# Kernel optimization log

Measured on AMD Instinct MI355X. Metric: run time of the kernel, lower is better.

The kernel has to match this reference:

```python
import jax, jax.numpy as jnp
import numpy as np

H = 4096      # hidden_size
NH = 32       # num query heads
NKV = 2       # multi_query_group_num (kv heads)
HD = 128      # head_dim
ROT = 64      # rotary_dim = head_dim // 2
B, S = 2, 2048
QKV = (NH + 2 * NKV) * HD  # 4608
BASE = 10000.0


def apply_rope(x, pos):
    """GPT-J style (non-neox, interleaved) rope on first ROT dims of head_dim.
    x: [B,S,n,HD], pos: [B,S] int."""
    half = ROT // 2  # 32 frequency pairs
    inv_freq = 1.0 / (BASE ** (jnp.arange(0, ROT, 2, dtype=jnp.float32) / ROT))  # [half]
    freqs = pos.astype(jnp.float32)[..., None] * inv_freq        # [B,S,half]
    cos = jnp.cos(freqs)[:, :, None, :]                          # [B,S,1,half]
    sin = jnp.sin(freqs)[:, :, None, :]
    xr, xp = x[..., :ROT], x[..., ROT:]
    x1 = xr[..., 0::2]   # [B,S,n,half]
    x2 = xr[..., 1::2]
    o1 = x1 * cos - x2 * sin
    o2 = x2 * cos + x1 * sin
    rot = jnp.stack([o1, o2], axis=-1).reshape(x.shape[:-1] + (ROT,))
    return jnp.concatenate([rot, xp], axis=-1)


def setup_inputs() -> dict:
    key = jax.random.key(0)
    k1, k2, k3, k4 = jax.random.split(key, 4)
    hidden_states = jax.random.normal(k1, (B, S, H), dtype=jnp.float32)
    position_ids = jnp.broadcast_to(jnp.arange(S, dtype=jnp.int64), (B, S))
    Wqkv = jax.random.normal(k2, (H, QKV), dtype=jnp.float32) * 0.02
    bqkv = jax.random.normal(k3, (QKV,), dtype=jnp.float32) * 0.02
    Wo = jax.random.normal(k4, (NH * HD, H), dtype=jnp.float32) * 0.02
    return {"hidden_states": hidden_states, "position_ids": position_ids,
            "Wqkv": Wqkv, "bqkv": bqkv, "Wo": Wo}


def reference(hidden_states, position_ids, Wqkv, bqkv, Wo):
    qkv = hidden_states @ Wqkv + bqkv                      # [B,S,QKV]
    q = qkv[..., : NH * HD].reshape(B, S, NH, HD)
    k = qkv[..., NH * HD : (NH + NKV) * HD].reshape(B, S, NKV, HD)
    v = qkv[..., (NH + NKV) * HD :].reshape(B, S, NKV, HD)

    q = apply_rope(q, position_ids)
    k = apply_rope(k, position_ids)

    # GQA: expand kv heads to match query heads
    rep = NH // NKV
    k = jnp.repeat(k, rep, axis=2)   # [B,S,NH,HD]
    v = jnp.repeat(v, rep, axis=2)

    scale = HD ** -0.5
    scores = jnp.einsum("bqhd,bkhd->bhqk", q, k) * scale   # [B,NH,S,S]
    causal = jnp.tril(jnp.ones((S, S), dtype=bool))
    scores = jnp.where(causal, scores, jnp.finfo(scores.dtype).min)
    probs = jax.nn.softmax(scores, axis=-1)
    ctx = jnp.einsum("bhqk,bkhd->bqhd", probs, v).reshape(B, S, NH * HD)
    return ctx @ Wo                                        # [B,S,H]
```

## Files before the change

### kernel.cpp

```cpp
#include <hip/hip_runtime.h>
#include <stdint.h>

#define B_    2
#define S_    2048
#define H_    4096
#define NH_   32
#define NKV_  2
#define HD_   128
#define ROT_  64
#define QKVD  4608
#define MROWS 4096

typedef __attribute__((ext_vector_type(8))) __bf16 bf16x8;
typedef __attribute__((ext_vector_type(4))) float f32x4;

__device__ __forceinline__ unsigned short f2bf(float f) {
    union { float f; unsigned u; } c; c.f = f;
    unsigned u = c.u;
    u += 0x7fffu + ((u >> 16) & 1u);
    return (unsigned short)(u >> 16);
}

__device__ __forceinline__ void gload_lds16(const void* g, void* l) {
    __builtin_amdgcn_global_load_lds(
        (__attribute__((address_space(1))) void*)g,
        (__attribute__((address_space(3))) void*)l, 16, 0, 0);
}

__global__ __launch_bounds__(256) void convert_bf16(const float* __restrict__ src,
                                                    unsigned short* __restrict__ dst,
                                                    int n4) {
    int i = blockIdx.x * 256 + threadIdx.x;
    if (i < n4) {
        f32x4 v = ((const f32x4*)src)[i];
        ushort4 o;
        o.x = f2bf(v[0]); o.y = f2bf(v[1]); o.z = f2bf(v[2]); o.w = f2bf(v[3]);
        ((ushort4*)dst)[i] = o;
    }
}

__global__ __launch_bounds__(256) void transpose_bf16(const float* __restrict__ src,
                                                      unsigned short* __restrict__ dst,
                                                      int K, int N) {
    __shared__ float tile[32][33];
    int n0 = blockIdx.x * 32, k0 = blockIdx.y * 32;
    int tx = threadIdx.x & 31, ty = threadIdx.x >> 5;
#pragma unroll
    for (int i = 0; i < 4; i++)
        tile[ty + i * 8][tx] = src[(size_t)(k0 + ty + i * 8) * N + n0 + tx];
    __syncthreads();
#pragma unroll
    for (int i = 0; i < 4; i++)
        dst[(size_t)(n0 + ty + i * 8) * K + k0 + tx] = f2bf(tile[tx][ty + i * 8]);
}


__device__ __forceinline__ void stage_half(const unsigned short* g,
                                           unsigned short* slot,
                                           int kt, int tid, int wave) {
    int ko = (kt < 64 ? kt : 63) << 6;
#pragma unroll
    for (int j = 0; j < 2; j++) {
        int li = j * 512 + tid;
        int r = li >> 3, s = li & 7;
        gload_lds16(g + ((size_t)r << 12) + ko + ((s ^ (r & 7)) << 3),
                    slot + (size_t)(j * 512 + wave * 64) * 8);
    }
}

template <int PAR, int MH>
__device__ __forceinline__ void lda_frags(const unsigned short* lds, bf16x8 (&af)[4][2],
                                          int wm, int lrow, int quad, int lw) {
    const unsigned short* p = lds + (PAR * 2 + MH) * 8192 + (wm * 64 + lrow) * 64;
#pragma unroll
    for (int mf = 0; mf < 4; mf++)
#pragma unroll
        for (int ks = 0; ks < 2; ks++)
            af[mf][ks] = *(const bf16x8*)(p + mf * 1024 + (((ks * 4 + quad) ^ lw) << 3));
}

template <int PAR, int NH>
__device__ __forceinline__ void ldb_frags(const unsigned short* lds, bf16x8 (&bf)[2][2],
                                          int wn, int lrow, int quad, int lw) {
    const unsigned short* p =
        lds + 32768 + (PAR * 2 + NH) * 8192 + (wn * 32 + lrow) * 64;
#pragma unroll
    for (int nf = 0; nf < 2; nf++)
#pragma unroll
        for (int ks = 0; ks < 2; ks++)
            bf[nf][ks] = *(const bf16x8*)(p + nf * 1024 + (((ks * 4 + quad) ^ lw) << 3));
}

template <int MH, int NH>
__device__ __forceinline__ void mfma_quad(f32x4 (&acc)[8][4], const bf16x8 (&af)[4][2],
                                          const bf16x8 (&bf)[2][2]) {
#pragma unroll
    for (int mf = 0; mf < 4; mf++)
#pragma unroll
        for (int nf = 0; nf < 2; nf++)
#pragma unroll
            for (int ks = 0; ks < 2; ks++)
                acc[MH * 4 + mf][NH * 2 + nf] = __builtin_amdgcn_mfma_f32_16x16x32_bf16(
                    af[mf][ks], bf[nf][ks], acc[MH * 4 + mf][NH * 2 + nf], 0, 0, 0);
}

#define MMPH(MH, NH, BF)                                   \
    __builtin_amdgcn_s_barrier();                          \
    asm volatile("s_waitcnt lgkmcnt(0)" ::: "memory");     \
    __builtin_amdgcn_s_setprio(1);                         \
    mfma_quad<MH, NH>(acc, af, BF);                        \
    __builtin_amdgcn_s_setprio(0);

template <int EPI, int N>
__global__ __launch_bounds__(512, 2) void gemm256(const unsigned short* __restrict__ A,
                                                  const unsigned short* __restrict__ BT,
                                                  const float* __restrict__ bias,
                                                  float* __restrict__ C,
                                                  unsigned short* __restrict__ Qb,
                                                  unsigned short* __restrict__ Kb,
                                                  unsigned short* __restrict__ Vb) {
    extern __shared__ unsigned short lds[];
    const int tid = threadIdx.x;
    const int lane = tid & 63, wave = tid >> 6;
    const int wm = wave >> 2, wn = wave & 3;
    const int quad = lane >> 4, lrow = lane & 15, lw = lrow & 7;
    const int m0 = blockIdx.y * 256, n0 = blockIdx.x * 256;
    const unsigned short* gA0 = A + ((size_t)m0 << 12);
    const unsigned short* gA1 = gA0 + ((size_t)128 << 12);
    const unsigned short* gB0 = BT + ((size_t)n0 << 12);
    const unsigned short* gB1 = gB0 + ((size_t)128 << 12);

    f32x4 acc[8][4];
#pragma unroll
    for (int i = 0; i < 8; i++)
#pragma unroll
        for (int j = 0; j < 4; j++) acc[i][j] = (f32x4){0.f, 0.f, 0.f, 0.f};
    bf16x8 af[4][2], bf0[2][2], bf1[2][2];

    stage_half(gA0, lds,                 0, tid, wave);
    stage_half(gB0, lds + 32768,         0, tid, wave);
    stage_half(gA1, lds + 8192,          0, tid, wave);
    stage_half(gB1, lds + 32768 + 8192,  0, tid, wave);
    stage_half(gA0, lds + 16384,         1, tid, wave);
    stage_half(gB0, lds + 32768 + 16384, 1, tid, wave);
    asm volatile("s_waitcnt vmcnt(4)" ::: "memory");
    __builtin_amdgcn_s_barrier();

#pragma unroll 1
    for (int i = 0; i < 32; ++i) {
        const int t0 = 2 * i;
        lda_frags<0, 0>(lds, af, wm, lrow, quad, lw);
        ldb_frags<0, 0>(lds, bf0, wn, lrow, quad, lw);
        stage_half(gA1, lds + 24576, t0 + 1, tid, wave);
        MMPH(0, 0, bf0);
        __builtin_amdgcn_s_barrier();
        ldb_frags<0, 1>(lds, bf1, wn, lrow, quad, lw);
        stage_half(gB1, lds + 32768 + 24576, t0 + 1, tid, wave);
        MMPH(0, 1, bf1);
        __builtin_amdgcn_s_barrier();
        lda_frags<0, 1>(lds, af, wm, lrow, quad, lw);
        stage_half(gA0, lds, t0 + 2, tid, wave);
        MMPH(1, 0, bf0);
        __builtin_amdgcn_s_barrier();
        stage_half(gB0, lds + 32768, t0 + 2, tid, wave);
        MMPH(1, 1, bf1);
        asm volatile("s_waitcnt vmcnt(4)" ::: "memory");
        __builtin_amdgcn_s_barrier();
        lda_frags<1, 0>(lds, af, wm, lrow, quad, lw);
        ldb_frags<1, 0>(lds, bf0, wn, lrow, quad, lw);
        stage_half(gA1, lds + 8192, t0 + 2, tid, wave);
        MMPH(0, 0, bf0);
        __builtin_amdgcn_s_barrier();
        ldb_frags<1, 1>(lds, bf1, wn, lrow, quad, lw);
        stage_half(gB1, lds + 32768 + 8192, t0 + 2, tid, wave);
        MMPH(0, 1, bf1);
        __builtin_amdgcn_s_barrier();
        lda_frags<1, 1>(lds, af, wm, lrow, quad, lw);
        stage_half(gA0, lds + 16384, t0 + 3, tid, wave);
        MMPH(1, 0, bf0);
        __builtin_amdgcn_s_barrier();
        stage_half(gB0, lds + 32768 + 16384, t0 + 3, tid, wave);
        MMPH(1, 1, bf1);
        asm volatile("s_waitcnt vmcnt(4)" ::: "memory");
        __builtin_amdgcn_s_barrier();
    }

    if constexpr (EPI == 0) {
#pragma unroll
        for (int mh = 0; mh < 2; mh++)
#pragma unroll
            for (int mf = 0; mf < 4; mf++) {
                int gm = m0 + mh * 128 + wm * 64 + mf * 16 + quad * 4;
#pragma unroll
                for (int nh = 0; nh < 2; nh++)
#pragma unroll
                    for (int nf = 0; nf < 2; nf++) {
                        int gn = n0 + nh * 128 + wn * 32 + nf * 16 + lrow;
#pragma unroll
                        for (int r = 0; r < 4; r++)
                            C[(size_t)(gm + r) * N + gn] = acc[mh * 4 + mf][nh * 2 + nf][r];
                    }
            }
    } else {
        const float QSCALE = 0.08838834764831843f * 1.4426950408889634f;
#pragma unroll
        for (int mh = 0; mh < 2; mh++)
#pragma unroll
            for (int mf = 0; mf < 4; mf++) {
                int gm = m0 + mh * 128 + wm * 64 + mf * 16 + quad * 4;
                int bb = gm >> 11;
                int srow = gm & (S_ - 1);
#pragma unroll
                for (int nh = 0; nh < 2; nh++)
#pragma unroll
                    for (int nf = 0; nf < 2; nf++) {
                        int colF = n0 + nh * 128 + wn * 32 + nf * 16 + lrow;
                        int head = colF >> 7, dcol = colF & 127;
                        float bv = bias[colF];
                        float vals[4];
#pragma unroll
                        for (int r = 0; r < 4; r++)
                            vals[r] = acc[mh * 4 + mf][nh * 2 + nf][r] + bv;
                        if (head < 34 && dcol < ROT_) {
                            int p = dcol >> 1;
                            float inv = exp2f(-(float)p * 0.41524101186092035f);
                            int odd = dcol & 1;
#pragma unroll
                            for (int r = 0; r < 4; r++) {
                                float partner = __shfl_xor(vals[r], 1);
                                float sn, cs;
                                __sincosf((float)(srow + r) * inv, &sn, &cs);
                                vals[r] = odd ? (vals[r] * cs + partner * sn)
                                              : (vals[r] * cs - partner * sn);
                            }
                        }
                        if (head < 32) {
                            unsigned short* dst =
                                Qb + ((size_t)(bb * NH_ + head) * S_ + srow) * HD_ + dcol;
#pragma unroll
                            for (int r = 0; r < 4; r++) dst[r * HD_] = f2bf(vals[r] * QSCALE);
                        } else if (head < 34) {
                            size_t base = ((size_t)(bb * NKV_ + head - 32) * S_ + srow) * HD_;
#pragma unroll
                            for (int r = 0; r < 4; r++)
                                Kb[base + r * HD_ + (((dcol >> 3) ^ ((srow + r) & 7)) << 3) +
                                   (dcol & 7)] = f2bf(vals[r]);
                        } else {
                            size_t base = ((size_t)(bb * NKV_ + head - 34) * HD_ + dcol) * S_;
#pragma unroll
                            for (int r = 0; r < 4; r++) {
                                int s = srow + r;
                                Vb[base + ((s >> 6) << 6) +
                                   ((((s >> 3) & 7) ^ (dcol & 7)) << 3) + (s & 7)] =
                                    f2bf(vals[r]);
                            }
                        }
                    }
            }
    }
}
#undef MMPH

__global__ __launch_bounds__(256, 4) void flash4(const unsigned short* __restrict__ Qb,
                                                 const unsigned short* __restrict__ Kb,
                                                 const unsigned short* __restrict__ Vb,
                                                 unsigned short* __restrict__ ctxb) {
    int pair = blockIdx.x;
    int h = blockIdx.y, b = blockIdx.z;
    int tid = threadIdx.x, lane = tid & 63, wave = tid >> 6;
    int quad = lane >> 4, lrow = lane & 15;
    int bkvh = b * NKV_ + (h >> 4);
    int lw3 = lrow & 7;

    __shared__ __align__(16) unsigned short Ks[64 * 128];
    __shared__ __align__(16) unsigned short Vt[128 * 64];
    __shared__ __align__(16) unsigned short Ps[4][16 * 64];

    const unsigned short* Kg = Kb + (size_t)bkvh * S_ * HD_;
    const unsigned short* Vg = Vb + (size_t)bkvh * HD_ * S_;

#pragma unroll 1
    for (int u = 0; u < 2; u++) {
        int qblk = u ? ((int)(S_ / 64) - 1 - pair) : pair;
        int q0 = qblk * 64 + wave * 16;

        bf16x8 qf[4];
        {
            const unsigned short* qr =
                Qb + ((size_t)(b * NH_ + h) * S_ + q0 + lrow) * HD_ + quad * 8;
#pragma unroll
            for (int c = 0; c < 4; c++) qf[c] = *(const bf16x8*)(qr + c * 32);
        }

        float m_i[4], l_i[4];
        f32x4 oacc[8];
#pragma unroll
        for (int r = 0; r < 4; r++) { m_i[r] = -1e30f; l_i[r] = 0.f; }
#pragma unroll
        for (int t = 0; t < 8; t++) oacc[t] = (f32x4){0.f, 0.f, 0.f, 0.f};

        int nkt = qblk + 1;
#pragma unroll 1
        for (int kt = 0; kt < nkt; kt++) {
            int ks0 = kt * 64;
            {
                const unsigned short* g =
                    Kg + (size_t)(ks0 + wave * 16 + (lane >> 4)) * HD_ + (lane & 15) * 8;
                unsigned short* l = &Ks[wave * 16 * 128];
#pragma unroll
                for (int i = 0; i < 4; i++)
                    gload_lds16(g + i * 4 * 128, l + i * 4 * 128);
            }
            {
                const unsigned short* g =
                    Vg + (size_t)(wave * 32 + (lane >> 3)) * S_ + ks0 + (lane & 7) * 8;
                unsigned short* l = &Vt[wave * 32 * 64];
#pragma unroll
                for (int i = 0; i < 4; i++)
                    gload_lds16(g + (size_t)i * 8 * S_, l + i * 8 * 64);
            }
            __syncthreads();

            if (ks0 <= q0 + 15) {
                f32x4 s[4];
#pragma unroll
                for (int n = 0; n < 4; n++) s[n] = (f32x4){0.f, 0.f, 0.f, 0.f};
#pragma unroll
                for (int kc = 0; kc < 4; kc++)
#pragma unroll
                    for (int n = 0; n < 4; n++) {
                        bf16x8 kf = *(const bf16x8*)
                            &Ks[(n * 16 + lrow) * 128 + (((kc * 4 + quad) ^ lw3) << 3)];
                        s[n] = __builtin_amdgcn_mfma_f32_16x16x32_bf16(qf[kc], kf, s[n],
                                                                       0, 0, 0);
                    }
                if (kt == nkt - 1) {
#pragma unroll
                    for (int n = 0; n < 4; n++)
#pragma unroll
                        for (int r = 0; r < 4; r++)
                            if (ks0 + n * 16 + lrow > q0 + quad * 4 + r)
                                s[n][r] = -1e30f;
                }
                float alpha[4];
#pragma unroll
                for (int r = 0; r < 4; r++) {
                    float mx = fmaxf(fmaxf(s[0][r], s[1][r]), fmaxf(s[2][r], s[3][r]));
                    mx = fmaxf(mx, __shfl_xor(mx, 1));
                    mx = fmaxf(mx, __shfl_xor(mx, 2));
                    mx = fmaxf(mx, __shfl_xor(mx, 4));
                    mx = fmaxf(mx, __shfl_xor(mx, 8));
                    float mn = fmaxf(m_i[r], mx);
                    alpha[r] = exp2f(m_i[r] - mn);
                    m_i[r] = mn;
                    float rs = 0.f;
#pragma unroll
                    for (int n = 0; n < 4; n++) {
                        s[n][r] = exp2f(s[n][r] - mn);
                        rs += s[n][r];
                    }
                    rs += __shfl_xor(rs, 1);
                    rs += __shfl_xor(rs, 2);
                    rs += __shfl_xor(rs, 4);
                    rs += __shfl_xor(rs, 8);
                    l_i[r] = l_i[r] * alpha[r] + rs;
                }
#pragma unroll
                for (int n = 0; n < 4; n++)
#pragma unroll
                    for (int r = 0; r < 4; r++) {
                        int rw = quad * 4 + r, col = n * 16 + lrow;
                        Ps[wave][rw * 64 + (((col >> 3) ^ (rw & 7)) << 3) + (col & 7)] =
                            f2bf(s[n][r]);
                    }
#pragma unroll
                for (int t = 0; t < 8; t++)
#pragma unroll
                    for (int r = 0; r < 4; r++) oacc[t][r] *= alpha[r];
                bf16x8 pf0 = *(const bf16x8*)&Ps[wave][lrow * 64 + ((quad ^ lw3) << 3)];
                bf16x8 pf1 = *(const bf16x8*)&Ps[wave][lrow * 64 + (((4 + quad) ^ lw3) << 3)];
#pragma unroll
                for (int t = 0; t < 8; t++) {
                    int dim = t * 16 + lrow;
                    bf16x8 v0 = *(const bf16x8*)&Vt[dim * 64 + ((quad ^ lw3) << 3)];
                    bf16x8 v1 = *(const bf16x8*)&Vt[dim * 64 + (((4 + quad) ^ lw3) << 3)];
                    oacc[t] = __builtin_amdgcn_mfma_f32_16x16x32_bf16(pf0, v0, oacc[t], 0, 0, 0);
                    oacc[t] = __builtin_amdgcn_mfma_f32_16x16x32_bf16(pf1, v1, oacc[t], 0, 0, 0);
                }
            }
            __syncthreads();
        }
        float inv[4];
#pragma unroll
        for (int r = 0; r < 4; r++) inv[r] = 1.f / l_i[r];
#pragma unroll
        for (int t = 0; t < 8; t++)
#pragma unroll
            for (int r = 0; r < 4; r++) {
                int q = q0 + quad * 4 + r;
                ctxb[(size_t)(b * S_ + q) * (NH_ * HD_) + h * HD_ + t * 16 + lrow] =
                    f2bf(oacc[t][r] * inv[r]);
            }
    }
}

extern "C" void kernel_launch(void* const* d_in, const int* in_sizes, int n_in,
                              void* d_out, int out_size, void* d_ws, size_t ws_size,
                              hipStream_t stream) {
    const float* hidden = (const float*)d_in[0];
    const float* Wqkv = (const float*)d_in[2];
    const float* bqkv = (const float*)d_in[3];
    const float* Wo   = (const float*)d_in[4];
    float* out = (float*)d_out;

    char* ws = (char*)d_ws;
    unsigned short* Xb    = (unsigned short*)ws;
    unsigned short* WqkvT = (unsigned short*)(ws + 33554432);
    unsigned short* Qb    = (unsigned short*)(ws + 71303168);
    unsigned short* Kb    = (unsigned short*)(ws + 104857600);
    unsigned short* Vb    = (unsigned short*)(ws + 106954752);
    unsigned short* ctxb  = (unsigned short*)(ws + 109051904);
    unsigned short* WoT   = Xb;

    convert_bf16<<<16384, 256, 0, stream>>>(hidden, Xb, (MROWS * H_) / 4);
    transpose_bf16<<<dim3(QKVD / 32, H_ / 32), 256, 0, stream>>>(Wqkv, WqkvT, H_, QKVD);
    gemm256<1, QKVD><<<dim3(QKVD / 256, MROWS / 256), 512, 131072, stream>>>(
        Xb, WqkvT, bqkv, nullptr, Qb, Kb, Vb);
    transpose_bf16<<<dim3(H_ / 32, H_ / 32), 256, 0, stream>>>(Wo, WoT, NH_ * HD_, H_);
    flash4<<<dim3(S_ / 128, NH_, B_), 256, 0, stream>>>(Qb, Kb, Vb, ctxb);
    gemm256<0, H_><<<dim3(H_ / 256, MROWS / 256), 512, 131072, stream>>>(
        ctxb, WoT, nullptr, out, nullptr, nullptr, nullptr);
}
```

Baseline: 711.2 us.

## Double-buffer 32-key K/V tiles in flash attention and remap GEMM block order

Rewrites the attention kernel to use 32-key tiles with double-buffered K/V loads into LDS. The next tile's load is issued before computing the current one, using vmcnt waits and raw barriers instead of __syncthreads, to overlap global loads with MFMA work. The V layout written by the QKV GEMM epilogue is changed to contiguous 32-key chunks with a new swizzle, so each tile loads as one contiguous 8 KB block. The GEMM also remaps block IDs in an XCD-aware order for cache locality. Smaller tiles double the loop iterations and the barrier count per query block.

```diff
diff --git a/kernel.cpp b/kernel.cpp
--- a/kernel.cpp
+++ b/kernel.cpp
@@ -124,7 +124,11 @@
     const int lane = tid & 63, wave = tid >> 6;
     const int wm = wave >> 2, wn = wave & 3;
     const int quad = lane >> 4, lrow = lane & 15, lw = lrow & 7;
-    const int m0 = blockIdx.y * 256, n0 = blockIdx.x * 256;
+    const int nx = gridDim.x;
+    const int bid0 = blockIdx.y * nx + blockIdx.x;
+    const int cpx = (nx * gridDim.y) >> 3;
+    const int bid = (bid0 & 7) * cpx + (bid0 >> 3);
+    const int m0 = (bid / nx) * 256, n0 = (bid % nx) * 256;
     const unsigned short* gA0 = A + ((size_t)m0 << 12);
     const unsigned short* gA1 = gA0 + ((size_t)128 << 12);
     const unsigned short* gB0 = BT + ((size_t)n0 << 12);
@@ -246,12 +250,12 @@
                                 Kb[base + r * HD_ + (((dcol >> 3) ^ ((srow + r) & 7)) << 3) +
                                    (dcol & 7)] = f2bf(vals[r]);
                         } else {
-                            size_t base = ((size_t)(bb * NKV_ + head - 34) * HD_ + dcol) * S_;
+                            size_t base = (size_t)(bb * NKV_ + head - 34) * S_ * HD_;
 #pragma unroll
                             for (int r = 0; r < 4; r++) {
                                 int s = srow + r;
-                                Vb[base + ((s >> 6) << 6) +
-                                   ((((s >> 3) & 7) ^ (dcol & 7)) << 3) + (s & 7)] =
+                                Vb[base + (size_t)(s >> 5) * 4096 + dcol * 32 +
+                                   ((((s >> 3) & 3) ^ ((dcol >> 1) & 3)) << 3) + (s & 7)] =
                                     f2bf(vals[r]);
                             }
                         }
@@ -261,7 +265,7 @@
 }
 #undef MMPH
 
-__global__ __launch_bounds__(256, 4) void flash4(const unsigned short* __restrict__ Qb,
+__global__ __launch_bounds__(256, 4) void flash5(const unsigned short* __restrict__ Qb,
                                                  const unsigned short* __restrict__ Kb,
                                                  const unsigned short* __restrict__ Vb,
                                                  unsigned short* __restrict__ ctxb) {
@@ -272,16 +276,16 @@
     int bkvh = b * NKV_ + (h >> 4);
     int lw3 = lrow & 7;
 
-    __shared__ __align__(16) unsigned short Ks[64 * 128];
-    __shared__ __align__(16) unsigned short Vt[128 * 64];
-    __shared__ __align__(16) unsigned short Ps[4][16 * 64];
+    __shared__ __align__(16) unsigned short Ks[2][32 * 128];
+    __shared__ __align__(16) unsigned short Vt[2][128 * 32];
+    __shared__ __align__(16) unsigned short Ps[4][16 * 32];
 
     const unsigned short* Kg = Kb + (size_t)bkvh * S_ * HD_;
-    const unsigned short* Vg = Vb + (size_t)bkvh * HD_ * S_;
+    const unsigned short* Vg = Vb + (size_t)bkvh * S_ * HD_;
 
 #pragma unroll 1
     for (int u = 0; u < 2; u++) {
-        int qblk = u ? ((int)(S_ / 64) - 1 - pair) : pair;
+        int qblk = u ? (31 - pair) : pair;
         int q0 = qblk * 64 + wave * 16;
 
         bf16x8 qf[4];
@@ -299,53 +303,60 @@
 #pragma unroll
         for (int t = 0; t < 8; t++) oacc[t] = (f32x4){0.f, 0.f, 0.f, 0.f};
 
-        int nkt = qblk + 1;
+        int nkt = 2 * qblk + 2;
+        gload_lds16(Kg + tid * 8, &Ks[0][tid * 8]);
+        gload_lds16(Kg + (256 + tid) * 8, &Ks[0][(256 + tid) * 8]);
+        gload_lds16(Vg + tid * 8, &Vt[0][tid * 8]);
+        gload_lds16(Vg + (256 + tid) * 8, &Vt[0][(256 + tid) * 8]);
+
 #pragma unroll 1
         for (int kt = 0; kt < nkt; kt++) {
-            int ks0 = kt * 64;
-            {
-                const unsigned short* g =
-                    Kg + (size_t)(ks0 + wave * 16 + (lane >> 4)) * HD_ + (lane & 15) * 8;
-                unsigned short* l = &Ks[wave * 16 * 128];
-#pragma unroll
-                for (int i = 0; i < 4; i++)
-                    gload_lds16(g + i * 4 * 128, l + i * 4 * 128);
+            int cur = kt & 1;
+            if (kt + 1 < nkt) {
+                const unsigned short* gk = Kg + (size_t)(kt + 1) * 4096;
+                const unsigned short* gv = Vg + (size_t)(kt + 1) * 4096;
+                int nb = cur ^ 1;
+                gload_lds16(gk + tid * 8, &Ks[nb][tid * 8]);
+                gload_lds16(gk + (256 + tid) * 8, &Ks[nb][(256 + tid) * 8]);
+                gload_lds16(gv + tid * 8, &Vt[nb][tid * 8]);
+                gload_lds16(gv + (256 + tid) * 8, &Vt[nb][(256 + tid) * 8]);
+                asm volatile("s_waitcnt vmcnt(4)" ::: "memory");
+            } else {
+                asm volatile("s_waitcnt vmcnt(0)" ::: "memory");
             }
-            {
-                const unsigned short* g =
-                    Vg + (size_t)(wave * 32 + (lane >> 3)) * S_ + ks0 + (lane & 7) * 8;
-                unsigned short* l = &Vt[wave * 32 * 64];
-#pragma unroll
-                for (int i = 0; i < 4; i++)
-                    gload_lds16(g + (size_t)i * 8 * S_, l + i * 8 * 64);
-            }
-            __syncthreads();
-
+            __builtin_amdgcn_s_barrier();
+            asm volatile("" ::: "memory");
+
+            int ks0 = kt * 32;
             if (ks0 <= q0 + 15) {
-                f32x4 s[4];
-#pragma unroll
-                for (int n = 0; n < 4; n++) s[n] = (f32x4){0.f, 0.f, 0.f, 0.f};
+                const unsigned short* KsB = &Ks[cur][0];
+                const unsigned short* VtB = &Vt[cur][0];
+                f32x4 s2[2];
+                s2[0] = (f32x4){0.f, 0.f, 0.f, 0.f};
+                s2[1] = (f32x4){0.f, 0.f, 0.f, 0.f};
+                __builtin_amdgcn_s_setprio(1);
 #pragma unroll
                 for (int kc = 0; kc < 4; kc++)
 #pragma unroll
-                    for (int n = 0; n < 4; n++) {
+                    for (int n = 0; n < 2; n++) {
                         bf16x8 kf = *(const bf16x8*)
-                            &Ks[(n * 16 + lrow) * 128 + (((kc * 4 + quad) ^ lw3) << 3)];
-                        s[n] = __builtin_amdgcn_mfma_f32_16x16x32_bf16(qf[kc], kf, s[n],
-                                                                       0, 0, 0);
+                            &KsB[(n * 16 + lrow) * 128 + (((kc * 4 + quad) ^ lw3) << 3)];
+                        s2[n] = __builtin_amdgcn_mfma_f32_16x16x32_bf16(qf[kc], kf, s2[n],
+                                                                        0, 0, 0);
                     }
-                if (kt == nkt - 1) {
-#pragma unroll
-                    for (int n = 0; n < 4; n++)
+                __builtin_amdgcn_s_setprio(0);
+                if (ks0 + 31 > q0) {
+#pragma unroll
+                    for (int n = 0; n < 2; n++)
 #pragma unroll
                         for (int r = 0; r < 4; r++)
                             if (ks0 + n * 16 + lrow > q0 + quad * 4 + r)
-                                s[n][r] = -1e30f;
+                                s2[n][r] = -1e30f;
                 }
                 float alpha[4];
 #pragma unroll
                 for (int r = 0; r < 4; r++) {
-                    float mx = fmaxf(fmaxf(s[0][r], s[1][r]), fmaxf(s[2][r], s[3][r]));
+                    float mx = fmaxf(s2[0][r], s2[1][r]);
                     mx = fmaxf(mx, __shfl_xor(mx, 1));
                     mx = fmaxf(mx, __shfl_xor(mx, 2));
                     mx = fmaxf(mx, __shfl_xor(mx, 4));
@@ -355,9 +366,9 @@
                     m_i[r] = mn;
                     float rs = 0.f;
 #pragma unroll
-                    for (int n = 0; n < 4; n++) {
-                        s[n][r] = exp2f(s[n][r] - mn);
-                        rs += s[n][r];
+                    for (int n = 0; n < 2; n++) {
+                        s2[n][r] = exp2f(s2[n][r] - mn);
+                        rs += s2[n][r];
                     }
                     rs += __shfl_xor(rs, 1);
                     rs += __shfl_xor(rs, 2);
@@ -366,29 +377,33 @@
                     l_i[r] = l_i[r] * alpha[r] + rs;
                 }
 #pragma unroll
-                for (int n = 0; n < 4; n++)
+                for (int n = 0; n < 2; n++)
 #pragma unroll
                     for (int r = 0; r < 4; r++) {
                         int rw = quad * 4 + r, col = n * 16 + lrow;
-                        Ps[wave][rw * 64 + (((col >> 3) ^ (rw & 7)) << 3) + (col & 7)] =
-                            f2bf(s[n][r]);
+                        Ps[wave][rw * 32 + ((((col >> 3) ^ ((rw >> 1) & 3)) << 3)) +
+                                 (col & 7)] = f2bf(s2[n][r]);
                     }
 #pragma unroll
                 for (int t = 0; t < 8; t++)
 #pragma unroll
                     for (int r = 0; r < 4; r++) oacc[t][r] *= alpha[r];
-                bf16x8 pf0 = *(const bf16x8*)&Ps[wave][lrow * 64 + ((quad ^ lw3) << 3)];
-                bf16x8 pf1 = *(const bf16x8*)&Ps[wave][lrow * 64 + (((4 + quad) ^ lw3) << 3)];
+                bf16x8 pf = *(const bf16x8*)
+                    &Ps[wave][lrow * 32 + ((quad ^ ((lrow >> 1) & 3)) << 3)];
+                __builtin_amdgcn_s_setprio(1);
 #pragma unroll
                 for (int t = 0; t < 8; t++) {
                     int dim = t * 16 + lrow;
-                    bf16x8 v0 = *(const bf16x8*)&Vt[dim * 64 + ((quad ^ lw3) << 3)];
-                    bf16x8 v1 = *(const bf16x8*)&Vt[dim * 64 + (((4 + quad) ^ lw3) << 3)];
-                    oacc[t] = __builtin_amdgcn_mfma_f32_16x16x32_bf16(pf0, v0, oacc[t], 0, 0, 0);
-                    oacc[t] = __builtin_amdgcn_mfma_f32_16x16x32_bf16(pf1, v1, oacc[t], 0, 0, 0);
+                    bf16x8 vf = *(const bf16x8*)
+                        &VtB[dim * 32 + ((quad ^ ((dim >> 1) & 3)) << 3)];
+                    oacc[t] = __builtin_amdgcn_mfma_f32_16x16x32_bf16(pf, vf, oacc[t],
+                                                                      0, 0, 0);
                 }
+                __builtin_amdgcn_s_setprio(0);
             }
-            __syncthreads();
+            asm volatile("s_waitcnt lgkmcnt(0)" ::: "memory");
+            __builtin_amdgcn_s_barrier();
+            asm volatile("" ::: "memory");
         }
         float inv[4];
 #pragma unroll
@@ -427,7 +442,7 @@
     gemm256<1, QKVD><<<dim3(QKVD / 256, MROWS / 256), 512, 131072, stream>>>(
         Xb, WqkvT, bqkv, nullptr, Qb, Kb, Vb);
     transpose_bf16<<<dim3(H_ / 32, H_ / 32), 256, 0, stream>>>(Wo, WoT, NH_ * HD_, H_);
-    flash4<<<dim3(S_ / 128, NH_, B_), 256, 0, stream>>>(Qb, Kb, Vb, ctxb);
+    flash5<<<dim3(S_ / 128, NH_, B_), 256, 0, stream>>>(Qb, Kb, Vb, ctxb);
     gemm256<0, H_><<<dim3(H_ / 256, MROWS / 256), 512, 131072, stream>>>(
         ctxb, WoT, nullptr, out, nullptr, nullptr, nullptr);
 }
```

Measured after the change: 783.8 us. +10.2%, slower.

## Rework flash attention to 32-row waves reading K/V directly from global

Applied to the files above, without the earlier changes.

The attention kernel now gives each wave 32 query rows in two 16-row groups that share each K and V fragment, doubling MFMA work per operand load. K and V are no longer staged in shared memory: waves read them straight from global memory, which removes the block-wide barriers and lets each wave stop at its own causal limit. To make those reads simple, the QKV GEMM epilogue writes K and V without swizzling, and V is written as a plain transposed layout with vectorized 4-element stores. MFMA sections are wrapped in s_setprio. The risks are higher register pressure (launch bounds drop to 2), reliance on L1/L2 for K/V reuse, and uneven work across waves in a block.

```diff
diff --git a/kernel.cpp b/kernel.cpp
--- a/kernel.cpp
+++ b/kernel.cpp
@@ -240,20 +240,18 @@
 #pragma unroll
                             for (int r = 0; r < 4; r++) dst[r * HD_] = f2bf(vals[r] * QSCALE);
                         } else if (head < 34) {
-                            size_t base = ((size_t)(bb * NKV_ + head - 32) * S_ + srow) * HD_;
+                            size_t base =
+                                ((size_t)(bb * NKV_ + head - 32) * S_ + srow) * HD_ + dcol;
 #pragma unroll
                             for (int r = 0; r < 4; r++)
-                                Kb[base + r * HD_ + (((dcol >> 3) ^ ((srow + r) & 7)) << 3) +
-                                   (dcol & 7)] = f2bf(vals[r]);
+                                Kb[base + r * HD_] = f2bf(vals[r]);
                         } else {
-                            size_t base = ((size_t)(bb * NKV_ + head - 34) * HD_ + dcol) * S_;
-#pragma unroll
-                            for (int r = 0; r < 4; r++) {
-                                int s = srow + r;
-                                Vb[base + ((s >> 6) << 6) +
-                                   ((((s >> 3) & 7) ^ (dcol & 7)) << 3) + (s & 7)] =
-                                    f2bf(vals[r]);
-                            }
+                            size_t base =
+                                ((size_t)(bb * NKV_ + head - 34) * HD_ + dcol) * S_ + srow;
+                            ushort4 vv;
+                            vv.x = f2bf(vals[0]); vv.y = f2bf(vals[1]);
+                            vv.z = f2bf(vals[2]); vv.w = f2bf(vals[3]);
+                            *(ushort4*)&Vb[base] = vv;
                         }
                     }
             }
@@ -261,7 +259,7 @@
 }
 #undef MMPH
 
-__global__ __launch_bounds__(256, 4) void flash4(const unsigned short* __restrict__ Qb,
+__global__ __launch_bounds__(256, 2) void flash6(const unsigned short* __restrict__ Qb,
                                                  const unsigned short* __restrict__ Kb,
                                                  const unsigned short* __restrict__ Vb,
                                                  unsigned short* __restrict__ ctxb) {
@@ -272,135 +270,146 @@
     int bkvh = b * NKV_ + (h >> 4);
     int lw3 = lrow & 7;
 
-    __shared__ __align__(16) unsigned short Ks[64 * 128];
-    __shared__ __align__(16) unsigned short Vt[128 * 64];
-    __shared__ __align__(16) unsigned short Ps[4][16 * 64];
+    __shared__ __align__(16) unsigned short Ps[4][32 * 64];
 
     const unsigned short* Kg = Kb + (size_t)bkvh * S_ * HD_;
-    const unsigned short* Vg = Vb + (size_t)bkvh * HD_ * S_;
+    const unsigned short* Vg = Vb + (size_t)bkvh * S_ * HD_;
 
 #pragma unroll 1
     for (int u = 0; u < 2; u++) {
-        int qblk = u ? ((int)(S_ / 64) - 1 - pair) : pair;
-        int q0 = qblk * 64 + wave * 16;
-
-        bf16x8 qf[4];
-        {
+        int qblk = u ? (15 - pair) : pair;
+        int q0 = qblk * 128 + wave * 32;
+
+        bf16x8 qf[2][4];
+#pragma unroll
+        for (int mg = 0; mg < 2; mg++) {
             const unsigned short* qr =
-                Qb + ((size_t)(b * NH_ + h) * S_ + q0 + lrow) * HD_ + quad * 8;
-#pragma unroll
-            for (int c = 0; c < 4; c++) qf[c] = *(const bf16x8*)(qr + c * 32);
+                Qb + ((size_t)(b * NH_ + h) * S_ + q0 + mg * 16 + lrow) * HD_ + quad * 8;
+#pragma unroll
+            for (int c = 0; c < 4; c++) qf[mg][c] = *(const bf16x8*)(qr + c * 32);
         }
 
-        float m_i[4], l_i[4];
-        f32x4 oacc[8];
-#pragma unroll
-        for (int r = 0; r < 4; r++) { m_i[r] = -1e30f; l_i[r] = 0.f; }
-#pragma unroll
-        for (int t = 0; t < 8; t++) oacc[t] = (f32x4){0.f, 0.f, 0.f, 0.f};
-
-        int nkt = qblk + 1;
+        float m_i[2][4], l_i[2][4];
+        f32x4 oacc[2][8];
+#pragma unroll
+        for (int mg = 0; mg < 2; mg++) {
+#pragma unroll
+            for (int r = 0; r < 4; r++) { m_i[mg][r] = -1e30f; l_i[mg][r] = 0.f; }
+#pragma unroll
+            for (int t = 0; t < 8; t++) oacc[mg][t] = (f32x4){0.f, 0.f, 0.f, 0.f};
+        }
+
+        int nkt = qblk * 2 + (wave >> 1) + 1;
 #pragma unroll 1
         for (int kt = 0; kt < nkt; kt++) {
             int ks0 = kt * 64;
-            {
-                const unsigned short* g =
-                    Kg + (size_t)(ks0 + wave * 16 + (lane >> 4)) * HD_ + (lane & 15) * 8;
-                unsigned short* l = &Ks[wave * 16 * 128];
-#pragma unroll
-                for (int i = 0; i < 4; i++)
-                    gload_lds16(g + i * 4 * 128, l + i * 4 * 128);
-            }
-            {
-                const unsigned short* g =
-                    Vg + (size_t)(wave * 32 + (lane >> 3)) * S_ + ks0 + (lane & 7) * 8;
-                unsigned short* l = &Vt[wave * 32 * 64];
-#pragma unroll
-                for (int i = 0; i < 4; i++)
-                    gload_lds16(g + (size_t)i * 8 * S_, l + i * 8 * 64);
-            }
-            __syncthreads();
-
-            if (ks0 <= q0 + 15) {
-                f32x4 s[4];
-#pragma unroll
-                for (int n = 0; n < 4; n++) s[n] = (f32x4){0.f, 0.f, 0.f, 0.f};
-#pragma unroll
-                for (int kc = 0; kc < 4; kc++)
-#pragma unroll
-                    for (int n = 0; n < 4; n++) {
-                        bf16x8 kf = *(const bf16x8*)
-                            &Ks[(n * 16 + lrow) * 128 + (((kc * 4 + quad) ^ lw3) << 3)];
-                        s[n] = __builtin_amdgcn_mfma_f32_16x16x32_bf16(qf[kc], kf, s[n],
-                                                                       0, 0, 0);
-                    }
-                if (kt == nkt - 1) {
+            f32x4 s[2][4];
+#pragma unroll
+            for (int mg = 0; mg < 2; mg++)
+#pragma unroll
+                for (int n = 0; n < 4; n++) s[mg][n] = (f32x4){0.f, 0.f, 0.f, 0.f};
+
+            __builtin_amdgcn_s_setprio(1);
+#pragma unroll
+            for (int n = 0; n < 4; n++)
+#pragma unroll
+                for (int kc = 0; kc < 4; kc++) {
+                    bf16x8 kf = *(const bf16x8*)
+                        &Kg[(size_t)(ks0 + n * 16 + lrow) * HD_ + ((kc * 4 + quad) << 3)];
+                    s[0][n] = __builtin_amdgcn_mfma_f32_16x16x32_bf16(qf[0][kc], kf,
+                                                                      s[0][n], 0, 0, 0);
+                    s[1][n] = __builtin_amdgcn_mfma_f32_16x16x32_bf16(qf[1][kc], kf,
+                                                                      s[1][n], 0, 0, 0);
+                }
+            __builtin_amdgcn_s_setprio(0);
+
+            if (ks0 + 63 > q0) {
+#pragma unroll
+                for (int mg = 0; mg < 2; mg++)
 #pragma unroll
                     for (int n = 0; n < 4; n++)
 #pragma unroll
                         for (int r = 0; r < 4; r++)
-                            if (ks0 + n * 16 + lrow > q0 + quad * 4 + r)
-                                s[n][r] = -1e30f;
-                }
+                            if (ks0 + n * 16 + lrow > q0 + mg * 16 + quad * 4 + r)
+                                s[mg][n][r] = -1e30f;
+            }
+
+#pragma unroll
+            for (int mg = 0; mg < 2; mg++) {
                 float alpha[4];
 #pragma unroll
                 for (int r = 0; r < 4; r++) {
-                    float mx = fmaxf(fmaxf(s[0][r], s[1][r]), fmaxf(s[2][r], s[3][r]));
+                    float mx = fmaxf(fmaxf(s[mg][0][r], s[mg][1][r]),
+                                     fmaxf(s[mg][2][r], s[mg][3][r]));
                     mx = fmaxf(mx, __shfl_xor(mx, 1));
                     mx = fmaxf(mx, __shfl_xor(mx, 2));
                     mx = fmaxf(mx, __shfl_xor(mx, 4));
                     mx = fmaxf(mx, __shfl_xor(mx, 8));
-                    float mn = fmaxf(m_i[r], mx);
-                    alpha[r] = exp2f(m_i[r] - mn);
-                    m_i[r] = mn;
+                    float mn = fmaxf(m_i[mg][r], mx);
+                    alpha[r] = exp2f(m_i[mg][r] - mn);
+                    m_i[mg][r] = mn;
                     float rs = 0.f;
 #pragma unroll
                     for (int n = 0; n < 4; n++) {
-                        s[n][r] = exp2f(s[n][r] - mn);
-                        rs += s[n][r];
+                        s[mg][n][r] = exp2f(s[mg][n][r] - mn);
+                        rs += s[mg][n][r];
                     }
                     rs += __shfl_xor(rs, 1);
                     rs += __shfl_xor(rs, 2);
                     rs += __shfl_xor(rs, 4);
                     rs += __shfl_xor(rs, 8);
-                    l_i[r] = l_i[r] * alpha[r] + rs;
+                    l_i[mg][r] = l_i[mg][r] * alpha[r] + rs;
                 }
 #pragma unroll
                 for (int n = 0; n < 4; n++)
 #pragma unroll
                     for (int r = 0; r < 4; r++) {
-                        int rw = quad * 4 + r, col = n * 16 + lrow;
+                        int rw = mg * 16 + quad * 4 + r, col = n * 16 + lrow;
                         Ps[wave][rw * 64 + (((col >> 3) ^ (rw & 7)) << 3) + (col & 7)] =
-                            f2bf(s[n][r]);
+                            f2bf(s[mg][n][r]);
                     }
 #pragma unroll
                 for (int t = 0; t < 8; t++)
 #pragma unroll
-                    for (int r = 0; r < 4; r++) oacc[t][r] *= alpha[r];
-                bf16x8 pf0 = *(const bf16x8*)&Ps[wave][lrow * 64 + ((quad ^ lw3) << 3)];
-                bf16x8 pf1 = *(const bf16x8*)&Ps[wave][lrow * 64 + (((4 + quad) ^ lw3) << 3)];
-#pragma unroll
-                for (int t = 0; t < 8; t++) {
-                    int dim = t * 16 + lrow;
-                    bf16x8 v0 = *(const bf16x8*)&Vt[dim * 64 + ((quad ^ lw3) << 3)];
-                    bf16x8 v1 = *(const bf16x8*)&Vt[dim * 64 + (((4 + quad) ^ lw3) << 3)];
-                    oacc[t] = __builtin_amdgcn_mfma_f32_16x16x32_bf16(pf0, v0, oacc[t], 0, 0, 0);
-                    oacc[t] = __builtin_amdgcn_mfma_f32_16x16x32_bf16(pf1, v1, oacc[t], 0, 0, 0);
+                    for (int r = 0; r < 4; r++) oacc[mg][t][r] *= alpha[r];
+            }
+
+            bf16x8 pA[2], pB[2];
+#pragma unroll
+            for (int mg = 0; mg < 2; mg++) {
+                int prow = mg * 16 + lrow;
+                pA[mg] = *(const bf16x8*)&Ps[wave][prow * 64 + ((quad ^ lw3) << 3)];
+                pB[mg] = *(const bf16x8*)&Ps[wave][prow * 64 + (((4 + quad) ^ lw3) << 3)];
+            }
+
+            __builtin_amdgcn_s_setprio(1);
+#pragma unroll
+            for (int t = 0; t < 8; t++) {
+                int dim = t * 16 + lrow;
+                bf16x8 v0 = *(const bf16x8*)&Vg[(size_t)dim * S_ + ks0 + quad * 8];
+                bf16x8 v1 = *(const bf16x8*)&Vg[(size_t)dim * S_ + ks0 + 32 + quad * 8];
+                oacc[0][t] = __builtin_amdgcn_mfma_f32_16x16x32_bf16(pA[0], v0, oacc[0][t], 0, 0, 0);
+                oacc[0][t] = __builtin_amdgcn_mfma_f32_16x16x32_bf16(pB[0], v1, oacc[0][t], 0, 0, 0);
+                oacc[1][t] = __builtin_amdgcn_mfma_f32_16x16x32_bf16(pA[1], v0, oacc[1][t], 0, 0, 0);
+                oacc[1][t] = __builtin_amdgcn_mfma_f32_16x16x32_bf16(pB[1], v1, oacc[1][t], 0, 0, 0);
+            }
+            __builtin_amdgcn_s_setprio(0);
+        }
+
+#pragma unroll
+        for (int mg = 0; mg < 2; mg++) {
+            float inv[4];
+#pragma unroll
+            for (int r = 0; r < 4; r++) inv[r] = 1.f / l_i[mg][r];
+#pragma unroll
+            for (int t = 0; t < 8; t++)
+#pragma unroll
+                for (int r = 0; r < 4; r++) {
+                    int q = q0 + mg * 16 + quad * 4 + r;
+                    ctxb[(size_t)(b * S_ + q) * (NH_ * HD_) + h * HD_ + t * 16 + lrow] =
+                        f2bf(oacc[mg][t][r] * inv[r]);
                 }
-            }
-            __syncthreads();
         }
-        float inv[4];
-#pragma unroll
-        for (int r = 0; r < 4; r++) inv[r] = 1.f / l_i[r];
-#pragma unroll
-        for (int t = 0; t < 8; t++)
-#pragma unroll
-            for (int r = 0; r < 4; r++) {
-                int q = q0 + quad * 4 + r;
-                ctxb[(size_t)(b * S_ + q) * (NH_ * HD_) + h * HD_ + t * 16 + lrow] =
-                    f2bf(oacc[t][r] * inv[r]);
-            }
     }
 }
 
@@ -427,7 +436,7 @@
     gemm256<1, QKVD><<<dim3(QKVD / 256, MROWS / 256), 512, 131072, stream>>>(
         Xb, WqkvT, bqkv, nullptr, Qb, Kb, Vb);
     transpose_bf16<<<dim3(H_ / 32, H_ / 32), 256, 0, stream>>>(Wo, WoT, NH_ * HD_, H_);
-    flash4<<<dim3(S_ / 128, NH_, B_), 256, 0, stream>>>(Qb, Kb, Vb, ctxb);
+    flash6<<<dim3(8, NH_, B_), 256, 0, stream>>>(Qb, Kb, Vb, ctxb);
     gemm256<0, H_><<<dim3(H_ / 256, MROWS / 256), 512, 131072, stream>>>(
         ctxb, WoT, nullptr, out, nullptr, nullptr, nullptr);
 }
```

Result: slower. 807.0 us (+13.5%).

## Double-buffer GEMM register fragments to prefetch LDS reads ahead of MFMA phases

Applied to the files above, without the earlier changes.

Restructures the GEMM main loop so A and B fragments are double-buffered in registers (AF0/AF1, BF0/BF1), with LDS reads for the next phase issued before the current phase's MFMAs. The explicit lgkmcnt(0) wait inside each phase is dropped and the vmcnt gates are moved. The aim is to hide LDS read latency behind MFMA work. In exchange it raises register pressure under the 512x2 launch bound and depends on compiler-inserted waits and a reordered barrier and vmcnt schedule for correctness.

```diff
diff --git a/kernel.cpp b/kernel.cpp
--- a/kernel.cpp
+++ b/kernel.cpp
@@ -79,6 +79,17 @@
             af[mf][ks] = *(const bf16x8*)(p + mf * 1024 + (((ks * 4 + quad) ^ lw) << 3));
 }
 
+template <int PAR, int MH, int HALF>
+__device__ __forceinline__ void lda_half(const unsigned short* lds, bf16x8 (&af)[4][2],
+                                         int wm, int lrow, int quad, int lw) {
+    const unsigned short* p = lds + (PAR * 2 + MH) * 8192 + (wm * 64 + lrow) * 64;
+#pragma unroll
+    for (int mf = HALF * 2; mf < HALF * 2 + 2; mf++)
+#pragma unroll
+        for (int ks = 0; ks < 2; ks++)
+            af[mf][ks] = *(const bf16x8*)(p + mf * 1024 + (((ks * 4 + quad) ^ lw) << 3));
+}
+
 template <int PAR, int NH>
 __device__ __forceinline__ void ldb_frags(const unsigned short* lds, bf16x8 (&bf)[2][2],
                                           int wn, int lrow, int quad, int lw) {
@@ -104,12 +115,14 @@
                     af[mf][ks], bf[nf][ks], acc[MH * 4 + mf][NH * 2 + nf], 0, 0, 0);
 }
 
-#define MMPH(MH, NH, BF)                                   \
+#define MMEXEC(MH, NH, AF, BF)                             \
     __builtin_amdgcn_s_barrier();                          \
-    asm volatile("s_waitcnt lgkmcnt(0)" ::: "memory");     \
     __builtin_amdgcn_s_setprio(1);                         \
-    mfma_quad<MH, NH>(acc, af, BF);                        \
-    __builtin_amdgcn_s_setprio(0);
+    mfma_quad<MH, NH>(acc, AF, BF);                        \
+    __builtin_amdgcn_s_setprio(0);                         \
+    __builtin_amdgcn_s_barrier();
+
+#define GATE4 asm volatile("s_waitcnt vmcnt(4)" ::: "memory");
 
 template <int EPI, int N>
 __global__ __launch_bounds__(512, 2) void gemm256(const unsigned short* __restrict__ A,
@@ -135,7 +148,7 @@
     for (int i = 0; i < 8; i++)
 #pragma unroll
         for (int j = 0; j < 4; j++) acc[i][j] = (f32x4){0.f, 0.f, 0.f, 0.f};
-    bf16x8 af[4][2], bf0[2][2], bf1[2][2];
+    bf16x8 AF0[4][2], AF1[4][2], BF0[2][2], BF1[2][2];
 
     stage_half(gA0, lds,                 0, tid, wave);
     stage_half(gB0, lds + 32768,         0, tid, wave);
@@ -143,46 +156,46 @@
     stage_half(gB1, lds + 32768 + 8192,  0, tid, wave);
     stage_half(gA0, lds + 16384,         1, tid, wave);
     stage_half(gB0, lds + 32768 + 16384, 1, tid, wave);
-    asm volatile("s_waitcnt vmcnt(4)" ::: "memory");
+    GATE4
     __builtin_amdgcn_s_barrier();
+    lda_frags<0, 0>(lds, AF0, wm, lrow, quad, lw);
+    ldb_frags<0, 0>(lds, BF0, wn, lrow, quad, lw);
 
 #pragma unroll 1
     for (int i = 0; i < 32; ++i) {
         const int t0 = 2 * i;
-        lda_frags<0, 0>(lds, af, wm, lrow, quad, lw);
-        ldb_frags<0, 0>(lds, bf0, wn, lrow, quad, lw);
+        lda_half<0, 1, 0>(lds, AF1, wm, lrow, quad, lw);
+        ldb_frags<0, 1>(lds, BF1, wn, lrow, quad, lw);
         stage_half(gA1, lds + 24576, t0 + 1, tid, wave);
-        MMPH(0, 0, bf0);
-        __builtin_amdgcn_s_barrier();
-        ldb_frags<0, 1>(lds, bf1, wn, lrow, quad, lw);
+        MMEXEC(0, 0, AF0, BF0)
+        lda_half<0, 1, 1>(lds, AF1, wm, lrow, quad, lw);
         stage_half(gB1, lds + 32768 + 24576, t0 + 1, tid, wave);
-        MMPH(0, 1, bf1);
-        __builtin_amdgcn_s_barrier();
-        lda_frags<0, 1>(lds, af, wm, lrow, quad, lw);
+        GATE4
+        MMEXEC(0, 1, AF0, BF1)
+        lda_half<1, 0, 0>(lds, AF0, wm, lrow, quad, lw);
         stage_half(gA0, lds, t0 + 2, tid, wave);
-        MMPH(1, 0, bf0);
-        __builtin_amdgcn_s_barrier();
+        MMEXEC(1, 0, AF1, BF0)
+        lda_half<1, 0, 1>(lds, AF0, wm, lrow, quad, lw);
+        ldb_frags<1, 0>(lds, BF0, wn, lrow, quad, lw);
         stage_half(gB0, lds + 32768, t0 + 2, tid, wave);
-        MMPH(1, 1, bf1);
-        asm volatile("s_waitcnt vmcnt(4)" ::: "memory");
-        __builtin_amdgcn_s_barrier();
-        lda_frags<1, 0>(lds, af, wm, lrow, quad, lw);
-        ldb_frags<1, 0>(lds, bf0, wn, lrow, quad, lw);
+        GATE4
+        MMEXEC(1, 1, AF1, BF1)
+        lda_half<1, 1, 0>(lds, AF1, wm, lrow, quad, lw);
+        ldb_frags<1, 1>(lds, BF1, wn, lrow, quad, lw);
         stage_half(gA1, lds + 8192, t0 + 2, tid, wave);
-        MMPH(0, 0, bf0);
-        __builtin_amdgcn_s_barrier();
-        ldb_frags<1, 1>(lds, bf1, wn, lrow, quad, lw);
+        MMEXEC(0, 0, AF0, BF0)
+        lda_half<1, 1, 1>(lds, AF1, wm, lrow, quad, lw);
         stage_half(gB1, lds + 32768 + 8192, t0 + 2, tid, wave);
-        MMPH(0, 1, bf1);
-        __builtin_amdgcn_s_barrier();
-        lda_frags<1, 1>(lds, af, wm, lrow, quad, lw);
+        GATE4
+        MMEXEC(0, 1, AF0, BF1)
+        lda_half<0, 0, 0>(lds, AF0, wm, lrow, quad, lw);
         stage_half(gA0, lds + 16384, t0 + 3, tid, wave);
-        MMPH(1, 0, bf0);
-        __builtin_amdgcn_s_barrier();
+        MMEXEC(1, 0, AF1, BF0)
+        lda_half<0, 0, 1>(lds, AF0, wm, lrow, quad, lw);
+        ldb_frags<0, 0>(lds, BF0, wn, lrow, quad, lw);
         stage_half(gB0, lds + 32768 + 16384, t0 + 3, tid, wave);
-        MMPH(1, 1, bf1);
-        asm volatile("s_waitcnt vmcnt(4)" ::: "memory");
-        __builtin_amdgcn_s_barrier();
+        GATE4
+        MMEXEC(1, 1, AF1, BF1)
     }
 
     if constexpr (EPI == 0) {
@@ -259,7 +272,8 @@
             }
     }
 }
-#undef MMPH
+#undef MMEXEC
+#undef GATE4
 
 __global__ __launch_bounds__(256, 4) void flash4(const unsigned short* __restrict__ Qb,
                                                  const unsigned short* __restrict__ Kb,
```

Measured after the change: 862.1 us. +21.2%, slower.
